# Kernel optimization log

Hardware: AMD Instinct MI355X
Metric: run time of the kernel (lower is better)

Reference implementation:

```python
import jax, jax.numpy as jnp
import numpy as np

IN_FEATURES = 1024
NUM_EXPERTS = 64
TOP_K = 2


def setup_inputs() -> dict:
    key = jax.random.key(0)
    kx, kw, kb = jax.random.split(key, 3)
    x = jax.random.normal(kx, (8, 4096, IN_FEATURES), dtype=jnp.float32)
    # nn.Linear init scale ~ 1/sqrt(in_features)
    bound = 1.0 / np.sqrt(IN_FEATURES)
    W = jax.random.uniform(kw, (NUM_EXPERTS, IN_FEATURES), dtype=jnp.float32, minval=-bound, maxval=bound)
    b = jax.random.uniform(kb, (NUM_EXPERTS,), dtype=jnp.float32, minval=-bound, maxval=bound)
    return {"x": x, "W": W, "b": b}


def reference(x, W, b):
    # logits: [B, S, E]
    logits = jnp.einsum("bsd,ed->bse", x, W) + b
    gates = jax.nn.softmax(logits, axis=-1)
    top_k_gates, top_k_indices = jax.lax.top_k(gates, TOP_K)
    return top_k_gates, top_k_indices
```

## Files before the change

kernel.cpp:

```cpp
#include <hip/hip_runtime.h>
#include <hip/hip_bf16.h>

#define D 1024
#define E 64
#define TPB 256
#define TOKS 64
#define KC 64
#define BROW 72

typedef __attribute__((ext_vector_type(8))) short bf16x8;
typedef __attribute__((ext_vector_type(4))) float f32x4;
typedef __attribute__((ext_vector_type(4))) unsigned short u16x4;

__device__ __forceinline__ unsigned short bf16_rne(float f) {
    unsigned u = __builtin_bit_cast(unsigned, f);
    u += 0x7fffu + ((u >> 16) & 1u);
    return (unsigned short)(u >> 16);
}
__device__ __forceinline__ float bf16_to_f(unsigned short h) {
    unsigned u = ((unsigned)h) << 16;
    return __builtin_bit_cast(float, u);
}
__device__ __forceinline__ void split_hi_lo(float v, unsigned short& h, unsigned short& l) {
    h = bf16_rne(v);
    l = bf16_rne(v - bf16_to_f(h));
}

__global__ __launch_bounds__(TPB) void router_kernel(
        const float* __restrict__ x, const float* __restrict__ W,
        const float* __restrict__ bias, float* __restrict__ out, int T) {
    __shared__ __align__(16) union SM {
        struct { unsigned short hi[E][BROW]; unsigned short lo[E][BROW]; } b;
        float ls[TOKS][E + 1];
    } sm;
    __shared__ float sbias[E];

    const int tid  = threadIdx.x;
    const int lane = tid & 63;
    const int wid  = tid >> 6;
    const int n    = lane & 15;
    const int q    = lane >> 4;
    const int t0   = blockIdx.x * TOKS;

    if (tid < E) sbias[tid] = bias[tid];

    f32x4 acc[4];
#pragma unroll
    for (int i = 0; i < 4; ++i) acc[i] = (f32x4){0.f, 0.f, 0.f, 0.f};

    const float* arow = x + (size_t)(t0 + wid * 16 + n) * D + q * 8;

    f32x4 wreg[4];
#pragma unroll
    for (int r = 0; r < 4; ++r) {
        int idx = r * TPB + tid;
        int e = idx >> 4, part = idx & 15;
        wreg[r] = *(const f32x4*)(W + e * D + part * 4);
    }
    f32x4 areg[4];
#pragma unroll
    for (int s = 0; s < 2; ++s) {
        areg[2 * s]     = *(const f32x4*)(arow + s * 32);
        areg[2 * s + 1] = *(const f32x4*)(arow + s * 32 + 4);
    }

    for (int kc = 0; kc < D; kc += KC) {
#pragma unroll
        for (int r = 0; r < 4; ++r) {
            int idx = r * TPB + tid;
            int e = idx >> 4, part = idx & 15;
            unsigned short h[4], l[4];
#pragma unroll
            for (int j = 0; j < 4; ++j) split_hi_lo(wreg[r][j], h[j], l[j]);
            *(u16x4*)&sm.b.hi[e][part * 4] = (u16x4){h[0], h[1], h[2], h[3]};
            *(u16x4*)&sm.b.lo[e][part * 4] = (u16x4){l[0], l[1], l[2], l[3]};
        }
        __syncthreads();

        int kn = (kc + KC) & (D - 1);
#pragma unroll
        for (int r = 0; r < 4; ++r) {
            int idx = r * TPB + tid;
            int e = idx >> 4, part = idx & 15;
            wreg[r] = *(const f32x4*)(W + e * D + kn + part * 4);
        }
        f32x4 anext[4];
#pragma unroll
        for (int s = 0; s < 2; ++s) {
            anext[2 * s]     = *(const f32x4*)(arow + kn + s * 32);
            anext[2 * s + 1] = *(const f32x4*)(arow + kn + s * 32 + 4);
        }

#pragma unroll
        for (int s = 0; s < 2; ++s) {
            unsigned short ah[8], al[8];
#pragma unroll
            for (int j = 0; j < 4; ++j) {
                split_hi_lo(areg[2 * s][j],     ah[j],     al[j]);
                split_hi_lo(areg[2 * s + 1][j], ah[4 + j], al[4 + j]);
            }
            bf16x8 ahv, alv;
#pragma unroll
            for (int j = 0; j < 8; ++j) { ahv[j] = (short)ah[j]; alv[j] = (short)al[j]; }
#pragma unroll
            for (int nt = 0; nt < 4; ++nt) {
                const bf16x8 bh = *(const bf16x8*)&sm.b.hi[nt * 16 + n][s * 32 + q * 8];
                const bf16x8 bl = *(const bf16x8*)&sm.b.lo[nt * 16 + n][s * 32 + q * 8];
                acc[nt] = __builtin_amdgcn_mfma_f32_16x16x32_bf16(ahv, bh, acc[nt], 0, 0, 0);
                acc[nt] = __builtin_amdgcn_mfma_f32_16x16x32_bf16(alv, bh, acc[nt], 0, 0, 0);
                acc[nt] = __builtin_amdgcn_mfma_f32_16x16x32_bf16(ahv, bl, acc[nt], 0, 0, 0);
            }
        }
#pragma unroll
        for (int i = 0; i < 4; ++i) areg[i] = anext[i];
        __syncthreads();
    }

#pragma unroll
    for (int nt = 0; nt < 4; ++nt) {
        int col = nt * 16 + n;
        float bv = sbias[col];
#pragma unroll
        for (int r = 0; r < 4; ++r) {
            sm.ls[wid * 16 + q * 4 + r][col] = acc[nt][r] + bv;
        }
    }
    __syncthreads();

    if (tid < TOKS) {
        float m1 = -3.4e38f, m2 = -3.4e38f;
        int i1 = 0, i2 = 0;
        for (int e = 0; e < E; ++e) {
            float v = sm.ls[tid][e];
            if (v > m1) { m2 = m1; i2 = i1; m1 = v; i1 = e; }
            else if (v > m2) { m2 = v; i2 = e; }
        }
        float Z = 0.f;
        for (int e = 0; e < E; ++e) Z += __expf(sm.ls[tid][e] - m1);
        float inv = 1.f / Z;
        int gt = t0 + tid;
        out[(size_t)gt * 2]     = inv;
        out[(size_t)gt * 2 + 1] = __expf(m2 - m1) * inv;
        float* oi = out + (size_t)T * 2;
        oi[(size_t)gt * 2]     = (float)i1;
        oi[(size_t)gt * 2 + 1] = (float)i2;
    }
}

extern "C" void kernel_launch(void* const* d_in, const int* in_sizes, int n_in,
                              void* d_out, int out_size, void* d_ws, size_t ws_size,
                              hipStream_t stream) {
    const float* x = (const float*)d_in[0];
    const float* W = (const float*)d_in[1];
    const float* b = (const float*)d_in[2];
    float* out = (float*)d_out;
    int T = in_sizes[0] / D;
    int blocks = T / TOKS;
    hipLaunchKernelGGL(router_kernel, dim3(blocks), dim3(TPB), 0, stream,
                       x, W, b, out, T);
}
```

Measured before the change: 206.2 us.

## Pre-split W into bf16 hi/lo fragment layout in a prep kernel, drop LDS

Adds a small prep kernel that converts W once per call into bf16 hi/lo pairs stored in the MFMA fragment order. The main kernel then loads B fragments straight from global memory (L2-resident) with register double-buffering, which removes the per-block W conversion, the LDS staging and the two barriers per K chunk. The activation split now uses the packed v_cvt_pk_bf16_f32 instruction with a 3-deep prefetch. The cost is an extra kernel launch and workspace traffic, plus higher register pressure under launch_bounds(256,2).

```diff
diff --git a/kernel.cpp b/kernel.cpp
--- a/kernel.cpp
+++ b/kernel.cpp
@@ -1,16 +1,15 @@
 #include <hip/hip_runtime.h>
-#include <hip/hip_bf16.h>
 
 #define D 1024
 #define E 64
 #define TPB 256
 #define TOKS 64
-#define KC 64
-#define BROW 72
+#define KSTEPS 32
 
 typedef __attribute__((ext_vector_type(8))) short bf16x8;
+typedef __attribute__((ext_vector_type(8))) unsigned short u16x8;
 typedef __attribute__((ext_vector_type(4))) float f32x4;
-typedef __attribute__((ext_vector_type(4))) unsigned short u16x4;
+typedef __attribute__((ext_vector_type(4))) unsigned int u32x4;
 
 __device__ __forceinline__ unsigned short bf16_rne(float f) {
     unsigned u = __builtin_bit_cast(unsigned, f);
@@ -21,19 +20,56 @@
     unsigned u = ((unsigned)h) << 16;
     return __builtin_bit_cast(float, u);
 }
-__device__ __forceinline__ void split_hi_lo(float v, unsigned short& h, unsigned short& l) {
-    h = bf16_rne(v);
-    l = bf16_rne(v - bf16_to_f(h));
+
+__device__ __forceinline__ unsigned cvt_pk_bf16(float a, float b) {
+    unsigned r;
+    asm("v_cvt_pk_bf16_f32 %0, %1, %2" : "=v"(r) : "v"(a), "v"(b));
+    return r;
 }
 
-__global__ __launch_bounds__(TPB) void router_kernel(
-        const float* __restrict__ x, const float* __restrict__ W,
+__device__ __forceinline__ void split8_rne(f32x4 a, f32x4 b, bf16x8& hv, bf16x8& lv) {
+    float e[8];
+#pragma unroll
+    for (int j = 0; j < 4; ++j) { e[j] = a[j]; e[4 + j] = b[j]; }
+    u32x4 hw, lw;
+#pragma unroll
+    for (int i = 0; i < 4; ++i) {
+        float e0 = e[2 * i], e1 = e[2 * i + 1];
+        unsigned hp = cvt_pk_bf16(e0, e1);
+        float f0 = __builtin_bit_cast(float, hp << 16);
+        float f1 = __builtin_bit_cast(float, hp & 0xffff0000u);
+        lw[i] = cvt_pk_bf16(e0 - f0, e1 - f1);
+        hw[i] = hp;
+    }
+    hv = __builtin_bit_cast(bf16x8, hw);
+    lv = __builtin_bit_cast(bf16x8, lw);
+}
+
+__global__ __launch_bounds__(TPB) void router_prep(
+        const float* __restrict__ W, unsigned short* __restrict__ Ws) {
+    int t = blockIdx.x * TPB + threadIdx.x;
+    int lane = t & 63;
+    int nt = (t >> 6) & 3;
+    int ks = t >> 8;
+    int n = lane & 15, q = lane >> 4;
+    const float* src = W + (size_t)(nt * 16 + n) * D + ks * 32 + q * 8;
+    u16x8 hv, lv;
+#pragma unroll
+    for (int j = 0; j < 8; ++j) {
+        float v = src[j];
+        unsigned short h = bf16_rne(v);
+        hv[j] = h;
+        lv[j] = bf16_rne(v - bf16_to_f(h));
+    }
+    size_t base = ((size_t)(ks * 8 + nt * 2) * 64 + lane) * 8;
+    *(u16x8*)(Ws + base)          = hv;
+    *(u16x8*)(Ws + base + 64 * 8) = lv;
+}
+
+__global__ __launch_bounds__(TPB, 2) void router_main(
+        const float* __restrict__ x, const unsigned short* __restrict__ Ws,
         const float* __restrict__ bias, float* __restrict__ out, int T) {
-    __shared__ __align__(16) union SM {
-        struct { unsigned short hi[E][BROW]; unsigned short lo[E][BROW]; } b;
-        float ls[TOKS][E + 1];
-    } sm;
-    __shared__ float sbias[E];
+    __shared__ __align__(16) float ls[TOKS][E + 1];
 
     const int tid  = threadIdx.x;
     const int lane = tid & 63;
@@ -42,88 +78,53 @@
     const int q    = lane >> 4;
     const int t0   = blockIdx.x * TOKS;
 
-    if (tid < E) sbias[tid] = bias[tid];
+    const float* arow = x + (size_t)(t0 + wid * 16 + n) * D + q * 8;
+    const bf16x8* bptr = (const bf16x8*)Ws + lane;
 
     f32x4 acc[4];
 #pragma unroll
     for (int i = 0; i < 4; ++i) acc[i] = (f32x4){0.f, 0.f, 0.f, 0.f};
 
-    const float* arow = x + (size_t)(t0 + wid * 16 + n) * D + q * 8;
-
-    f32x4 wreg[4];
+    f32x4 abuf[4][2];
+    bf16x8 bbuf[2][8];
 #pragma unroll
-    for (int r = 0; r < 4; ++r) {
-        int idx = r * TPB + tid;
-        int e = idx >> 4, part = idx & 15;
-        wreg[r] = *(const f32x4*)(W + e * D + part * 4);
+    for (int p = 0; p < 3; ++p) {
+        abuf[p][0] = *(const f32x4*)(arow + p * 32);
+        abuf[p][1] = *(const f32x4*)(arow + p * 32 + 4);
     }
-    f32x4 areg[4];
 #pragma unroll
-    for (int s = 0; s < 2; ++s) {
-        areg[2 * s]     = *(const f32x4*)(arow + s * 32);
-        areg[2 * s + 1] = *(const f32x4*)(arow + s * 32 + 4);
-    }
-
-    for (int kc = 0; kc < D; kc += KC) {
-#pragma unroll
-        for (int r = 0; r < 4; ++r) {
-            int idx = r * TPB + tid;
-            int e = idx >> 4, part = idx & 15;
-            unsigned short h[4], l[4];
-#pragma unroll
-            for (int j = 0; j < 4; ++j) split_hi_lo(wreg[r][j], h[j], l[j]);
-            *(u16x4*)&sm.b.hi[e][part * 4] = (u16x4){h[0], h[1], h[2], h[3]};
-            *(u16x4*)&sm.b.lo[e][part * 4] = (u16x4){l[0], l[1], l[2], l[3]};
-        }
-        __syncthreads();
-
-        int kn = (kc + KC) & (D - 1);
-#pragma unroll
-        for (int r = 0; r < 4; ++r) {
-            int idx = r * TPB + tid;
-            int e = idx >> 4, part = idx & 15;
-            wreg[r] = *(const f32x4*)(W + e * D + kn + part * 4);
-        }
-        f32x4 anext[4];
-#pragma unroll
-        for (int s = 0; s < 2; ++s) {
-            anext[2 * s]     = *(const f32x4*)(arow + kn + s * 32);
-            anext[2 * s + 1] = *(const f32x4*)(arow + kn + s * 32 + 4);
-        }
+    for (int f = 0; f < 8; ++f) bbuf[0][f] = bptr[f * 64];
 
 #pragma unroll
-        for (int s = 0; s < 2; ++s) {
-            unsigned short ah[8], al[8];
+    for (int ks = 0; ks < KSTEPS; ++ks) {
+        if (ks + 3 < KSTEPS) {
+            abuf[(ks + 3) & 3][0] = *(const f32x4*)(arow + (ks + 3) * 32);
+            abuf[(ks + 3) & 3][1] = *(const f32x4*)(arow + (ks + 3) * 32 + 4);
+        }
+        if (ks + 1 < KSTEPS) {
 #pragma unroll
-            for (int j = 0; j < 4; ++j) {
-                split_hi_lo(areg[2 * s][j],     ah[j],     al[j]);
-                split_hi_lo(areg[2 * s + 1][j], ah[4 + j], al[4 + j]);
-            }
-            bf16x8 ahv, alv;
+            for (int f = 0; f < 8; ++f)
+                bbuf[(ks + 1) & 1][f] = bptr[((ks + 1) * 8 + f) * 64];
+        }
+        bf16x8 ah, al;
+        split8_rne(abuf[ks & 3][0], abuf[ks & 3][1], ah, al);
 #pragma unroll
-            for (int j = 0; j < 8; ++j) { ahv[j] = (short)ah[j]; alv[j] = (short)al[j]; }
-#pragma unroll
-            for (int nt = 0; nt < 4; ++nt) {
-                const bf16x8 bh = *(const bf16x8*)&sm.b.hi[nt * 16 + n][s * 32 + q * 8];
-                const bf16x8 bl = *(const bf16x8*)&sm.b.lo[nt * 16 + n][s * 32 + q * 8];
-                acc[nt] = __builtin_amdgcn_mfma_f32_16x16x32_bf16(ahv, bh, acc[nt], 0, 0, 0);
-                acc[nt] = __builtin_amdgcn_mfma_f32_16x16x32_bf16(alv, bh, acc[nt], 0, 0, 0);
-                acc[nt] = __builtin_amdgcn_mfma_f32_16x16x32_bf16(ahv, bl, acc[nt], 0, 0, 0);
-            }
+        for (int nt = 0; nt < 4; ++nt) {
+            const bf16x8 bh = bbuf[ks & 1][nt * 2];
+            const bf16x8 bl = bbuf[ks & 1][nt * 2 + 1];
+            acc[nt] = __builtin_amdgcn_mfma_f32_16x16x32_bf16(ah, bh, acc[nt], 0, 0, 0);
+            acc[nt] = __builtin_amdgcn_mfma_f32_16x16x32_bf16(al, bh, acc[nt], 0, 0, 0);
+            acc[nt] = __builtin_amdgcn_mfma_f32_16x16x32_bf16(ah, bl, acc[nt], 0, 0, 0);
         }
-#pragma unroll
-        for (int i = 0; i < 4; ++i) areg[i] = anext[i];
-        __syncthreads();
     }
 
 #pragma unroll
     for (int nt = 0; nt < 4; ++nt) {
         int col = nt * 16 + n;
-        float bv = sbias[col];
+        float bv = bias[col];
 #pragma unroll
-        for (int r = 0; r < 4; ++r) {
-            sm.ls[wid * 16 + q * 4 + r][col] = acc[nt][r] + bv;
-        }
+        for (int r = 0; r < 4; ++r)
+            ls[wid * 16 + q * 4 + r][col] = acc[nt][r] + bv;
     }
     __syncthreads();
 
@@ -131,12 +132,12 @@
         float m1 = -3.4e38f, m2 = -3.4e38f;
         int i1 = 0, i2 = 0;
         for (int e = 0; e < E; ++e) {
-            float v = sm.ls[tid][e];
+            float v = ls[tid][e];
             if (v > m1) { m2 = m1; i2 = i1; m1 = v; i1 = e; }
             else if (v > m2) { m2 = v; i2 = e; }
         }
         float Z = 0.f;
-        for (int e = 0; e < E; ++e) Z += __expf(sm.ls[tid][e] - m1);
+        for (int e = 0; e < E; ++e) Z += __expf(ls[tid][e] - m1);
         float inv = 1.f / Z;
         int gt = t0 + tid;
         out[(size_t)gt * 2]     = inv;
@@ -154,8 +155,9 @@
     const float* W = (const float*)d_in[1];
     const float* b = (const float*)d_in[2];
     float* out = (float*)d_out;
+    unsigned short* Ws = (unsigned short*)d_ws;
     int T = in_sizes[0] / D;
-    int blocks = T / TOKS;
-    hipLaunchKernelGGL(router_kernel, dim3(blocks), dim3(TPB), 0, stream,
-                       x, W, b, out, T);
+    hipLaunchKernelGGL(router_prep, dim3(32), dim3(TPB), 0, stream, W, Ws);
+    hipLaunchKernelGGL(router_main, dim3(T / TOKS), dim3(TPB), 0, stream,
+                       x, Ws, b, out, T);
 }
```

New measurement: 226.3 us. 1.1x slower.
